# Kernel optimization log

Measured on AMD Instinct MI355X. Metric: run time of the kernel, lower is better.

Reference implementation:

```python
import jax, jax.numpy as jnp
import numpy as np

NUM_NODES = 100000
IN_CH = 128
OUT_CH = 64
NUM_EDGES = 1000000


def setup_inputs() -> dict:
    key = jax.random.key(0)
    ks = jax.random.split(key, 16)

    x = jax.random.normal(ks[0], (NUM_NODES, IN_CH), dtype=jnp.float32)

    def make_edges(k_src, k_tgt, k_w):
        src = jax.random.randint(k_src, (NUM_EDGES,), 0, NUM_NODES, dtype=jnp.int32)
        # tf.math.segment_sum requires sorted segment ids -> sort targets
        tgt = jnp.sort(jax.random.randint(k_tgt, (NUM_EDGES,), 0, NUM_NODES, dtype=jnp.int32))
        ei = jnp.stack([src, tgt], axis=0)  # (2, E)
        ew = jax.random.uniform(k_w, (NUM_EDGES,), dtype=jnp.float32)
        return ei, ew

    edge_index_in, edge_weight_in = make_edges(ks[1], ks[2], ks[3])
    edge_index_out, edge_weight_out = make_edges(ks[4], ks[5], ks[6])

    glorot = (6.0 / (IN_CH + OUT_CH)) ** 0.5
    W_main_in = jax.random.uniform(ks[7], (IN_CH, OUT_CH), minval=-glorot, maxval=glorot, dtype=jnp.float32)
    W_main_out = jax.random.uniform(ks[8], (IN_CH, OUT_CH), minval=-glorot, maxval=glorot, dtype=jnp.float32)
    W_shared = jax.random.uniform(ks[9], (IN_CH, OUT_CH), minval=-glorot, maxval=glorot, dtype=jnp.float32)

    bias_main_in = jnp.zeros((OUT_CH,), dtype=jnp.float32)
    bias_main_out = jnp.zeros((OUT_CH,), dtype=jnp.float32)
    bias_shared_in = jnp.zeros((OUT_CH,), dtype=jnp.float32)
    bias_shared_out = jnp.zeros((OUT_CH,), dtype=jnp.float32)

    C_in_vec = jnp.ones((NUM_NODES, 1), dtype=jnp.float32)
    C_out_vec = jnp.ones((NUM_NODES, 1), dtype=jnp.float32)

    return {
        "x": x,
        "W_main_in": W_main_in,
        "W_main_out": W_main_out,
        "W_shared": W_shared,
        "bias_main_in": bias_main_in,
        "bias_main_out": bias_main_out,
        "bias_shared_in": bias_shared_in,
        "bias_shared_out": bias_shared_out,
        "C_in_vec": C_in_vec,
        "C_out_vec": C_out_vec,
        "edge_index_in": edge_index_in,
        "edge_weight_in": edge_weight_in,
        "edge_index_out": edge_index_out,
        "edge_weight_out": edge_weight_out,
    }


def _propagate(h, edge_index, edge_weight, num_nodes):
    # gather messages from source nodes, scale by edge weight, sum into targets
    src = edge_index[0]
    tgt = edge_index[1]
    msgs = h[src] * edge_weight[:, None]  # (E, OUT_CH)
    return jax.ops.segment_sum(msgs, tgt, num_segments=num_nodes)  # (N, OUT_CH)


def reference(x, W_main_in, W_main_out, W_shared,
              bias_main_in, bias_main_out, bias_shared_in, bias_shared_out,
              C_in_vec, C_out_vec,
              edge_index_in, edge_weight_in, edge_index_out, edge_weight_out):
    n = x.shape[0]
    h_main_in = _propagate(x @ W_main_in, edge_index_in, edge_weight_in, n)
    h_shared_in = _propagate(x @ W_shared, edge_index_in, edge_weight_in, n)
    ic_combined = h_main_in + bias_main_in + (h_shared_in + bias_shared_in)

    h_main_out = _propagate(x @ W_main_out, edge_index_out, edge_weight_out, n)
    h_shared_out = _propagate(x @ W_shared, edge_index_out, edge_weight_out, n)
    oc_combined = h_main_out + bias_main_out + (h_shared_out + bias_shared_out)

    return C_in_vec * ic_combined + C_out_vec * oc_combined
```

## Files before the change

kernel.cpp:

```cpp
#include <hip/hip_runtime.h>

#define IN_CH   128
#define OUT_CH  64
#define M_TILE  128
#define XS_PITCH 136

typedef __attribute__((ext_vector_type(8))) short short8;
typedef __attribute__((ext_vector_type(4))) float floatx4;

__device__ __forceinline__ unsigned short f2bf(float f) {
    union { float f; unsigned u; } v; v.f = f;
    unsigned r = v.u + 0x7fffu + ((v.u >> 16) & 1u);
    return (unsigned short)(r >> 16);
}
__device__ __forceinline__ float bfl(unsigned u) {
    return __uint_as_float(u << 16);
}
__device__ __forceinline__ float bfh(unsigned u) {
    return __uint_as_float(u & 0xffff0000u);
}

__global__ void prep_kernel(const int* __restrict__ tgtIn,
                            const int* __restrict__ tgtOut,
                            const float* __restrict__ Wmi,
                            const float* __restrict__ Wmo,
                            const float* __restrict__ Wsh,
                            int* __restrict__ rpIn,
                            int* __restrict__ rpOut,
                            unsigned short* __restrict__ WcT,
                            int n_nodes, int neIn, int neOut)
{
    int i = blockIdx.x * blockDim.x + threadIdx.x;
    int half = n_nodes + 1;
    if (i < 2 * half) {
        const int* tgt; int* rp; int t; int ne;
        if (i < half) { tgt = tgtIn;  rp = rpIn;  t = i;        ne = neIn; }
        else          { tgt = tgtOut; rp = rpOut; t = i - half; ne = neOut; }
        int lo = 0, hi = ne;
        while (lo < hi) {
            int mid = (lo + hi) >> 1;
            if (tgt[mid] < t) lo = mid + 1; else hi = mid;
        }
        rp[t] = lo;
    } else {
        int j = i - 2 * half;
        if (j < 2 * OUT_CH * IN_CH) {
            int n = j >> 7, k = j & 127;
            float m = (n < OUT_CH) ? Wmi[k * OUT_CH + n]
                                   : Wmo[k * OUT_CH + (n - OUT_CH)];
            float s = Wsh[k * OUT_CH + (n & (OUT_CH - 1))];
            WcT[n * IN_CH + k] = f2bf(m + s);
        }
    }
}

__global__ __launch_bounds__(256, 3)
void gemm_kernel(const float* __restrict__ x,
                 const unsigned short* __restrict__ WcT,
                 unsigned short* __restrict__ Abf,
                 unsigned short* __restrict__ Bbf,
                 int n_nodes)
{
    __shared__ unsigned short Xs[M_TILE][XS_PITCH];

    const int tid  = threadIdx.x;
    const int w    = tid >> 6;
    const int lane = tid & 63;
    const int l15  = lane & 15;
    const int quad = lane >> 4;
    const long long node0 = (long long)blockIdx.x * M_TILE;

    short8 bfrag[4][2];
#pragma unroll
    for (int ks = 0; ks < 4; ++ks)
#pragma unroll
        for (int ni = 0; ni < 2; ++ni)
            bfrag[ks][ni] = *(const short8*)&WcT[(w * 32 + ni * 16 + l15) * IN_CH
                                                 + ks * 32 + quad * 8];

    {
        const float4* x4 = (const float4*)x;
        for (int i = tid; i < M_TILE * (IN_CH / 4); i += 256) {
            int row = i >> 5, c4 = i & 31;
            long long node = node0 + row;
            float4 v = make_float4(0.f, 0.f, 0.f, 0.f);
            if (node < n_nodes) v = x4[node * (IN_CH / 4) + c4];
            uint2 p;
            p.x = ((unsigned)f2bf(v.y) << 16) | f2bf(v.x);
            p.y = ((unsigned)f2bf(v.w) << 16) | f2bf(v.z);
            *(uint2*)&Xs[row][c4 * 4] = p;
        }
    }
    __syncthreads();

    floatx4 acc[8][2];
#pragma unroll
    for (int mi = 0; mi < 8; ++mi)
#pragma unroll
        for (int ni = 0; ni < 2; ++ni)
            acc[mi][ni] = (floatx4){0.f, 0.f, 0.f, 0.f};

#pragma unroll
    for (int ks = 0; ks < 4; ++ks) {
        const int k0 = ks * 32 + quad * 8;
#pragma unroll
        for (int mi = 0; mi < 8; ++mi) {
            short8 a = *(const short8*)&Xs[mi * 16 + l15][k0];
            acc[mi][0] = __builtin_amdgcn_mfma_f32_16x16x32_bf16(a, bfrag[ks][0], acc[mi][0], 0, 0, 0);
            acc[mi][1] = __builtin_amdgcn_mfma_f32_16x16x32_bf16(a, bfrag[ks][1], acc[mi][1], 0, 0, 0);
        }
    }

    unsigned short* Hout = (w < 2) ? Abf : Bbf;
    const int colb = (w & 1) * 32;
#pragma unroll
    for (int mi = 0; mi < 8; ++mi)
#pragma unroll
        for (int ni = 0; ni < 2; ++ni)
#pragma unroll
            for (int r = 0; r < 4; ++r) {
                long long row = node0 + mi * 16 + quad * 4 + r;
                if (row < n_nodes)
                    Hout[row * OUT_CH + colb + ni * 16 + l15] = f2bf(acc[mi][ni][r]);
            }
}

__global__ __launch_bounds__(256)
void prop_kernel(const unsigned short* __restrict__ H,
                 const int* __restrict__ rpIn, const int* __restrict__ rpOut,
                 const int* __restrict__ srcIn, const float* __restrict__ ewIn,
                 const int* __restrict__ srcOut, const float* __restrict__ ewOut,
                 const float* __restrict__ bmi, const float* __restrict__ bmo,
                 const float* __restrict__ bsi, const float* __restrict__ bso,
                 const float* __restrict__ Cin, const float* __restrict__ Cout,
                 float* __restrict__ out, int n_nodes, int neIn, int neOut)
{
    const int lane = threadIdx.x & 63;
    const int wv   = threadIdx.x >> 6;
    const int q    = lane >> 4;
    const int ql   = lane & 15;
    const int ch4  = ql * 4;
    const int qb   = lane & 48;

    const unsigned short* Hq = H + ch4;

    const int t = ((int)blockIdx.x * 4 + wv) * 4 + q;
    const bool valid = (t < n_nodes);
    const int tc = valid ? t : 0;

    const int Boff = n_nodes * OUT_CH;

    int ei0 = rpIn[tc],  ei1 = rpIn[tc + 1];
    int eo0 = rpOut[tc], eo1 = rpOut[tc + 1];
    int dIn  = ei1 - ei0;
    int len  = valid ? (dIn + (eo1 - eo0)) : 0;
    float ci = Cin[tc], co = Cout[tc];

    int l0 = __shfl(len, 0),  l1 = __shfl(len, 16);
    int l2 = __shfl(len, 32), l3 = __shfl(len, 48);
    int maxlen = __builtin_amdgcn_readfirstlane(max(max(l0, l1), max(l2, l3)));

    float a0 = 0.f, a1 = 0.f, a2 = 0.f, a3 = 0.f;

    for (int p = 0; p < maxlen; p += 16) {
        int j = p + ql;
        int iIn  = min(ei0 + max(0, min(j, dIn - 1)), neIn - 1);
        int jo   = j - dIn;
        int iOut = min(eo0 + max(0, jo), neOut - 1);
        int   sIn  = srcIn[iIn];
        float wIn  = ewIn[iIn];
        int   sOut = srcOut[iOut];
        float wOut = ewOut[iOut];
        bool inSeg  = (j < dIn);
        bool anySeg = (j < len);
        int   rowb = inSeg ? (sIn * OUT_CH) : (sOut * OUT_CH + Boff);
        rowb = anySeg ? rowb : 0;
        float wj = inSeg ? (ci * wIn) : (anySeg ? (co * wOut) : 0.f);

        int m = min(16, maxlen - p);
        for (int j2 = 0; j2 < m; j2 += 4) {
            int   r0 = __shfl(rowb, qb + j2 + 0);
            int   r1 = __shfl(rowb, qb + j2 + 1);
            int   r2 = __shfl(rowb, qb + j2 + 2);
            int   r3 = __shfl(rowb, qb + j2 + 3);
            float w0 = __shfl(wj, qb + j2 + 0);
            float w1 = __shfl(wj, qb + j2 + 1);
            float w2 = __shfl(wj, qb + j2 + 2);
            float w3 = __shfl(wj, qb + j2 + 3);
            uint2 u0 = *(const uint2*)(Hq + r0);
            uint2 u1 = *(const uint2*)(Hq + r1);
            uint2 u2 = *(const uint2*)(Hq + r2);
            uint2 u3 = *(const uint2*)(Hq + r3);
            a0 += w0 * bfl(u0.x); a1 += w0 * bfh(u0.x);
            a2 += w0 * bfl(u0.y); a3 += w0 * bfh(u0.y);
            a0 += w1 * bfl(u1.x); a1 += w1 * bfh(u1.x);
            a2 += w1 * bfl(u1.y); a3 += w1 * bfh(u1.y);
            a0 += w2 * bfl(u2.x); a1 += w2 * bfh(u2.x);
            a2 += w2 * bfl(u2.y); a3 += w2 * bfh(u2.y);
            a0 += w3 * bfl(u3.x); a1 += w3 * bfh(u3.x);
            a2 += w3 * bfl(u3.y); a3 += w3 * bfh(u3.y);
        }
    }

    if (valid) {
        float4 o;
        o.x = a0 + ci * (bmi[ch4 + 0] + bsi[ch4 + 0]) + co * (bmo[ch4 + 0] + bso[ch4 + 0]);
        o.y = a1 + ci * (bmi[ch4 + 1] + bsi[ch4 + 1]) + co * (bmo[ch4 + 1] + bso[ch4 + 1]);
        o.z = a2 + ci * (bmi[ch4 + 2] + bsi[ch4 + 2]) + co * (bmo[ch4 + 2] + bso[ch4 + 2]);
        o.w = a3 + ci * (bmi[ch4 + 3] + bsi[ch4 + 3]) + co * (bmo[ch4 + 3] + bso[ch4 + 3]);
        *(float4*)(out + (long long)t * OUT_CH + ch4) = o;
    }
}

extern "C" void kernel_launch(void* const* d_in, const int* in_sizes, int n_in,
                              void* d_out, int out_size, void* d_ws, size_t ws_size,
                              hipStream_t stream)
{
    const float* x    = (const float*)d_in[0];
    const float* Wmi  = (const float*)d_in[1];
    const float* Wmo  = (const float*)d_in[2];
    const float* Wsh  = (const float*)d_in[3];
    const float* bmi  = (const float*)d_in[4];
    const float* bmo  = (const float*)d_in[5];
    const float* bsi  = (const float*)d_in[6];
    const float* bso  = (const float*)d_in[7];
    const float* Cin  = (const float*)d_in[8];
    const float* Cout = (const float*)d_in[9];
    const int*   eiIn  = (const int*)d_in[10];
    const float* ewIn  = (const float*)d_in[11];
    const int*   eiOut = (const int*)d_in[12];
    const float* ewOut = (const float*)d_in[13];

    const int n_nodes = in_sizes[0] / IN_CH;
    const int neIn  = in_sizes[11];
    const int neOut = in_sizes[13];

    const int* srcIn  = eiIn;
    const int* tgtIn  = eiIn + neIn;
    const int* srcOut = eiOut;
    const int* tgtOut = eiOut + neOut;

    char* ws = (char*)d_ws;
    size_t NH = (size_t)n_nodes * OUT_CH * sizeof(unsigned short);
    unsigned short* Abf = (unsigned short*)ws;
    unsigned short* Bbf = (unsigned short*)(ws + NH);
    int* rpIn  = (int*)(ws + 2 * NH);
    int* rpOut = rpIn + (n_nodes + 1);
    unsigned short* WcT = (unsigned short*)(rpOut + (n_nodes + 1));

    int prep_threads = 2 * (n_nodes + 1) + 2 * OUT_CH * IN_CH;
    prep_kernel<<<(prep_threads + 255) / 256, 256, 0, stream>>>(
        tgtIn, tgtOut, Wmi, Wmo, Wsh, rpIn, rpOut, WcT, n_nodes, neIn, neOut);

    int gblocks = (n_nodes + M_TILE - 1) / M_TILE;
    gemm_kernel<<<gblocks, 256, 0, stream>>>(x, WcT, Abf, Bbf, n_nodes);

    int pblocks = (n_nodes + 15) / 16;
    prop_kernel<<<pblocks, 256, 0, stream>>>(
        Abf, rpIn, rpOut, srcIn, ewIn, srcOut, ewOut,
        bmi, bmo, bsi, bso, Cin, Cout, (float*)d_out, n_nodes, neIn, neOut);
}
```

Before: 188.8 us.

## Process 8 nodes per wave with 16-byte gathers and prefetched edge data

```diff
diff --git a/kernel.cpp b/kernel.cpp
--- a/kernel.cpp
+++ b/kernel.cpp
@@ -137,14 +137,14 @@
 {
     const int lane = threadIdx.x & 63;
     const int wv   = threadIdx.x >> 6;
-    const int q    = lane >> 4;
-    const int ql   = lane & 15;
-    const int ch4  = ql * 4;
-    const int qb   = lane & 48;
-
-    const unsigned short* Hq = H + ch4;
-
-    const int t = ((int)blockIdx.x * 4 + wv) * 4 + q;
+    const int e    = lane >> 3;
+    const int el   = lane & 7;
+    const int ch8  = el * 8;
+    const int eb   = lane & 56;
+
+    const unsigned short* Hq = H + ch8;
+
+    const int t = ((int)blockIdx.x * 4 + wv) * 8 + e;
     const bool valid = (t < n_nodes);
     const int tc = valid ? t : 0;
 
@@ -156,59 +156,84 @@
     int len  = valid ? (dIn + (eo1 - eo0)) : 0;
     float ci = Cin[tc], co = Cout[tc];
 
-    int l0 = __shfl(len, 0),  l1 = __shfl(len, 16);
-    int l2 = __shfl(len, 32), l3 = __shfl(len, 48);
-    int maxlen = __builtin_amdgcn_readfirstlane(max(max(l0, l1), max(l2, l3)));
+    int ml = len;
+    ml = max(ml, __shfl_xor(ml, 8));
+    ml = max(ml, __shfl_xor(ml, 16));
+    ml = max(ml, __shfl_xor(ml, 32));
+    const int maxlen = __builtin_amdgcn_readfirstlane(ml);
 
     float a0 = 0.f, a1 = 0.f, a2 = 0.f, a3 = 0.f;
-
-    for (int p = 0; p < maxlen; p += 16) {
-        int j = p + ql;
+    float a4 = 0.f, a5 = 0.f, a6 = 0.f, a7 = 0.f;
+
+    auto load_raw = [&](int j, int& sI, float& wI, int& sO, float& wO) {
         int iIn  = min(ei0 + max(0, min(j, dIn - 1)), neIn - 1);
         int jo   = j - dIn;
         int iOut = min(eo0 + max(0, jo), neOut - 1);
-        int   sIn  = srcIn[iIn];
-        float wIn  = ewIn[iIn];
-        int   sOut = srcOut[iOut];
-        float wOut = ewOut[iOut];
+        sI = srcIn[iIn];  wI = ewIn[iIn];
+        sO = srcOut[iOut]; wO = ewOut[iOut];
+    };
+
+    int   sI, sO;  float wI, wO;
+    load_raw(el, sI, wI, sO, wO);
+
+    for (int p = 0; p < maxlen; p += 8) {
+        int j = p + el;
         bool inSeg  = (j < dIn);
         bool anySeg = (j < len);
-        int   rowb = inSeg ? (sIn * OUT_CH) : (sOut * OUT_CH + Boff);
+        int   rowb = inSeg ? (sI * OUT_CH) : (sO * OUT_CH + Boff);
         rowb = anySeg ? rowb : 0;
-        float wj = inSeg ? (ci * wIn) : (anySeg ? (co * wOut) : 0.f);
-
-        int m = min(16, maxlen - p);
-        for (int j2 = 0; j2 < m; j2 += 4) {
-            int   r0 = __shfl(rowb, qb + j2 + 0);
-            int   r1 = __shfl(rowb, qb + j2 + 1);
-            int   r2 = __shfl(rowb, qb + j2 + 2);
-            int   r3 = __shfl(rowb, qb + j2 + 3);
-            float w0 = __shfl(wj, qb + j2 + 0);
-            float w1 = __shfl(wj, qb + j2 + 1);
-            float w2 = __shfl(wj, qb + j2 + 2);
-            float w3 = __shfl(wj, qb + j2 + 3);
-            uint2 u0 = *(const uint2*)(Hq + r0);
-            uint2 u1 = *(const uint2*)(Hq + r1);
-            uint2 u2 = *(const uint2*)(Hq + r2);
-            uint2 u3 = *(const uint2*)(Hq + r3);
-            a0 += w0 * bfl(u0.x); a1 += w0 * bfh(u0.x);
-            a2 += w0 * bfl(u0.y); a3 += w0 * bfh(u0.y);
-            a0 += w1 * bfl(u1.x); a1 += w1 * bfh(u1.x);
-            a2 += w1 * bfl(u1.y); a3 += w1 * bfh(u1.y);
-            a0 += w2 * bfl(u2.x); a1 += w2 * bfh(u2.x);
-            a2 += w2 * bfl(u2.y); a3 += w2 * bfh(u2.y);
-            a0 += w3 * bfl(u3.x); a1 += w3 * bfh(u3.x);
-            a2 += w3 * bfl(u3.y); a3 += w3 * bfh(u3.y);
-        }
+        float wj = inSeg ? (ci * wI) : (anySeg ? (co * wO) : 0.f);
+
+        if (p + 8 < maxlen)
+            load_raw(p + 8 + el, sI, wI, sO, wO);
+
+        int   r0 = __shfl(rowb, eb + 0), r1 = __shfl(rowb, eb + 1);
+        int   r2 = __shfl(rowb, eb + 2), r3 = __shfl(rowb, eb + 3);
+        int   r4 = __shfl(rowb, eb + 4), r5 = __shfl(rowb, eb + 5);
+        int   r6 = __shfl(rowb, eb + 6), r7 = __shfl(rowb, eb + 7);
+        float w0 = __shfl(wj, eb + 0), w1 = __shfl(wj, eb + 1);
+        float w2 = __shfl(wj, eb + 2), w3 = __shfl(wj, eb + 3);
+        float w4 = __shfl(wj, eb + 4), w5 = __shfl(wj, eb + 5);
+        float w6 = __shfl(wj, eb + 6), w7 = __shfl(wj, eb + 7);
+        uint4 u0 = *(const uint4*)(Hq + r0);
+        uint4 u1 = *(const uint4*)(Hq + r1);
+        uint4 u2 = *(const uint4*)(Hq + r2);
+        uint4 u3 = *(const uint4*)(Hq + r3);
+        uint4 u4 = *(const uint4*)(Hq + r4);
+        uint4 u5 = *(const uint4*)(Hq + r5);
+        uint4 u6 = *(const uint4*)(Hq + r6);
+        uint4 u7 = *(const uint4*)(Hq + r7);
+        a0 += w0 * bfl(u0.x); a1 += w0 * bfh(u0.x); a2 += w0 * bfl(u0.y); a3 += w0 * bfh(u0.y);
+        a4 += w0 * bfl(u0.z); a5 += w0 * bfh(u0.z); a6 += w0 * bfl(u0.w); a7 += w0 * bfh(u0.w);
+        a0 += w1 * bfl(u1.x); a1 += w1 * bfh(u1.x); a2 += w1 * bfl(u1.y); a3 += w1 * bfh(u1.y);
+        a4 += w1 * bfl(u1.z); a5 += w1 * bfh(u1.z); a6 += w1 * bfl(u1.w); a7 += w1 * bfh(u1.w);
+        a0 += w2 * bfl(u2.x); a1 += w2 * bfh(u2.x); a2 += w2 * bfl(u2.y); a3 += w2 * bfh(u2.y);
+        a4 += w2 * bfl(u2.z); a5 += w2 * bfh(u2.z); a6 += w2 * bfl(u2.w); a7 += w2 * bfh(u2.w);
+        a0 += w3 * bfl(u3.x); a1 += w3 * bfh(u3.x); a2 += w3 * bfl(u3.y); a3 += w3 * bfh(u3.y);
+        a4 += w3 * bfl(u3.z); a5 += w3 * bfh(u3.z); a6 += w3 * bfl(u3.w); a7 += w3 * bfh(u3.w);
+        a0 += w4 * bfl(u4.x); a1 += w4 * bfh(u4.x); a2 += w4 * bfl(u4.y); a3 += w4 * bfh(u4.y);
+        a4 += w4 * bfl(u4.z); a5 += w4 * bfh(u4.z); a6 += w4 * bfl(u4.w); a7 += w4 * bfh(u4.w);
+        a0 += w5 * bfl(u5.x); a1 += w5 * bfh(u5.x); a2 += w5 * bfl(u5.y); a3 += w5 * bfh(u5.y);
+        a4 += w5 * bfl(u5.z); a5 += w5 * bfh(u5.z); a6 += w5 * bfl(u5.w); a7 += w5 * bfh(u5.w);
+        a0 += w6 * bfl(u6.x); a1 += w6 * bfh(u6.x); a2 += w6 * bfl(u6.y); a3 += w6 * bfh(u6.y);
+        a4 += w6 * bfl(u6.z); a5 += w6 * bfh(u6.z); a6 += w6 * bfl(u6.w); a7 += w6 * bfh(u6.w);
+        a0 += w7 * bfl(u7.x); a1 += w7 * bfh(u7.x); a2 += w7 * bfl(u7.y); a3 += w7 * bfh(u7.y);
+        a4 += w7 * bfl(u7.z); a5 += w7 * bfh(u7.z); a6 += w7 * bfl(u7.w); a7 += w7 * bfh(u7.w);
     }
 
     if (valid) {
-        float4 o;
-        o.x = a0 + ci * (bmi[ch4 + 0] + bsi[ch4 + 0]) + co * (bmo[ch4 + 0] + bso[ch4 + 0]);
-        o.y = a1 + ci * (bmi[ch4 + 1] + bsi[ch4 + 1]) + co * (bmo[ch4 + 1] + bso[ch4 + 1]);
-        o.z = a2 + ci * (bmi[ch4 + 2] + bsi[ch4 + 2]) + co * (bmo[ch4 + 2] + bso[ch4 + 2]);
-        o.w = a3 + ci * (bmi[ch4 + 3] + bsi[ch4 + 3]) + co * (bmo[ch4 + 3] + bso[ch4 + 3]);
-        *(float4*)(out + (long long)t * OUT_CH + ch4) = o;
+        float4 o0, o1;
+        o0.x = a0 + ci * (bmi[ch8 + 0] + bsi[ch8 + 0]) + co * (bmo[ch8 + 0] + bso[ch8 + 0]);
+        o0.y = a1 + ci * (bmi[ch8 + 1] + bsi[ch8 + 1]) + co * (bmo[ch8 + 1] + bso[ch8 + 1]);
+        o0.z = a2 + ci * (bmi[ch8 + 2] + bsi[ch8 + 2]) + co * (bmo[ch8 + 2] + bso[ch8 + 2]);
+        o0.w = a3 + ci * (bmi[ch8 + 3] + bsi[ch8 + 3]) + co * (bmo[ch8 + 3] + bso[ch8 + 3]);
+        o1.x = a4 + ci * (bmi[ch8 + 4] + bsi[ch8 + 4]) + co * (bmo[ch8 + 4] + bso[ch8 + 4]);
+        o1.y = a5 + ci * (bmi[ch8 + 5] + bsi[ch8 + 5]) + co * (bmo[ch8 + 5] + bso[ch8 + 5]);
+        o1.z = a6 + ci * (bmi[ch8 + 6] + bsi[ch8 + 6]) + co * (bmo[ch8 + 6] + bso[ch8 + 6]);
+        o1.w = a7 + ci * (bmi[ch8 + 7] + bsi[ch8 + 7]) + co * (bmo[ch8 + 7] + bso[ch8 + 7]);
+        float* ob = out + (long long)t * OUT_CH + ch8;
+        *(float4*)ob = o0;
+        *(float4*)(ob + 4) = o1;
     }
 }
 
@@ -255,7 +280,7 @@
     int gblocks = (n_nodes + M_TILE - 1) / M_TILE;
     gemm_kernel<<<gblocks, 256, 0, stream>>>(x, WcT, Abf, Bbf, n_nodes);
 
-    int pblocks = (n_nodes + 15) / 16;
+    int pblocks = (n_nodes + 31) / 32;
     prop_kernel<<<pblocks, 256, 0, stream>>>(
         Abf, rpIn, rpOut, srcIn, ewIn, srcOut, ewOut,
         bmi, bmo, bsi, bso, Cin, Cout, (float*)d_out, n_nodes, neIn, neOut);
```

Result: no change. 187.7 us (-0.6%).
